# Performance work log

Measured on AMD Instinct MI355X. Metric: run time of the kernel, lower is better.

Reference implementation:

```python
import jax, jax.numpy as jnp
import numpy as np

B, L, D, NH, NITEMS = 256, 200, 128, 2, 100000
HD = D // NH
LAMB = 0.6
NEG = -1e9

_PARAM_SHAPES = dict(
    item_emb=(NITEMS, D), pos_emb=(L, D),
    W_ei=(D, D), b_ei=(D,), W_eo=(D, D), b_eo=(D,), b_iah=(D,), b_oah=(D,),
    w_ih=(3 * D, 2 * D), b_ih=(3 * D,), w_hh=(3 * D, D), b_hh=(3 * D,),
    ln1_g=(D,), ln1_b=(D,),
    Wq=(D, D), bq=(D,), Wk=(D, D), bk=(D,), Wv=(D, D), bv=(D,), Wo=(D, D), bo=(D,),
    ln2_g=(D,), ln2_b=(D,), W1=(D, D), b1=(D,), W2=(D, D), b2=(D,),
    lnf_g=(D,), lnf_b=(D,),
)


def setup_inputs() -> dict:
    key = jax.random.key(0)
    ks = jax.random.split(key, len(_PARAM_SHAPES) + 2)
    stdv = 1.0 / np.sqrt(D)  # GCSAN._init_weights: uniform(-stdv, stdv) on ALL params
    p = {}
    for i, (name, shp) in enumerate(_PARAM_SHAPES.items()):
        p[name] = jax.random.uniform(ks[i], shp, jnp.float32, -stdv, stdv)
    lens = jax.random.randint(ks[-2], (B,), L // 4, L + 1)
    vals = jax.random.randint(ks[-1], (B, L), 1, NITEMS)
    # trailing zero padding, as the original break-on-zero loop assumes
    seqs = jnp.where(jnp.arange(L)[None, :] < lens[:, None], vals, 0).astype(jnp.int32)
    p['seqs'] = seqs
    p['lens'] = lens.astype(jnp.int32)
    return p


def _ln(x, g, b):
    mu = x.mean(-1, keepdims=True)
    var = ((x - mu) ** 2).mean(-1, keepdims=True)
    return (x - mu) / jnp.sqrt(var + 1e-5) * g + b


def _build_graph(seqs):
    # Vectorized replacement of _get_slice (per-row np.unique + adjacency build)
    def per_row(seq):
        s = jnp.sort(seq)
        first = jnp.concatenate([jnp.ones((1,), bool), s[1:] != s[:-1]])
        pos = jnp.cumsum(first) - 1  # compaction target of each first-occurrence
        items = jnp.zeros((L,), seq.dtype).at[jnp.where(first, pos, L)].set(s, mode='drop')
        n_u = first.sum()
        search = jnp.where(jnp.arange(L) < n_u, items, jnp.iinfo(jnp.int32).max)
        alias = jnp.searchsorted(search, seq).astype(jnp.int32)
        return items, alias
    items, alias = jax.vmap(per_row)(seqs)
    valid = seqs[:, 1:] > 0  # edge (i -> i+1) exists until first pad
    u = jnp.where(valid, alias[:, :-1], L)  # route masked edges to dummy row L
    v = jnp.where(valid, alias[:, 1:], L)
    bidx = jnp.arange(B)[:, None]
    uA = jnp.zeros((B, L + 1, L + 1), jnp.float32).at[bidx, u, v].set(1.0)[:, :L, :L]
    in_deg = jnp.maximum(uA.sum(1), 1.0)
    out_deg = jnp.maximum(uA.sum(2), 1.0)
    A_in = jnp.swapaxes(uA, 1, 2) / in_deg[:, :, None]   # A[i,j] = uA[j,i]/in_deg[i]
    A_out = uA / out_deg[:, :, None]                     # A[i,k] = uA[i,k]/out_deg[i]
    return alias, jnp.concatenate([A_in, A_out], axis=2), items  # A: [B, L, 2L]


def reference(item_emb, pos_emb, W_ei, b_ei, W_eo, b_eo, b_iah, b_oah,
              w_ih, b_ih, w_hh, b_hh, ln1_g, ln1_b, Wq, bq, Wk, bk, Wv, bv,
              Wo, bo, ln2_g, ln2_b, W1, b1, W2, b2, lnf_g, lnf_b, seqs, lens):
    alias, A, items = _build_graph(seqs)
    hidden = item_emb[items]  # [B, L, D]
    # SR-GNN gated cell, step = n_layers = 1
    for _ in range(1):
        h_in = jnp.einsum('bij,bjd->bid', A[:, :, :L], hidden @ W_ei.T + b_ei) + b_iah
        h_out = jnp.einsum('bij,bjd->bid', A[:, :, L:], hidden @ W_eo.T + b_eo) + b_oah
        gi = jnp.concatenate([h_in, h_out], -1) @ w_ih.T + b_ih
        gh = hidden @ w_hh.T + b_hh
        i_r, i_i, i_n = jnp.split(gi, 3, -1)
        h_r, h_i, h_n = jnp.split(gh, 3, -1)
        r = jax.nn.sigmoid(i_r + h_r)
        z = jax.nn.sigmoid(i_i + h_i)
        ng = jnp.tanh(i_n + r * h_n)
        hidden = ng + z * (hidden - ng)
    bidx = jnp.arange(B)
    seq_hidden = hidden[bidx[:, None], alias]  # alias-gather back to sequence order
    last_idx = lens - 1
    ht = seq_hidden[bidx, last_idx]
    x = seq_hidden + pos_emb[None, :, :]
    tl_mask = (seqs > 0)[:, :, None].astype(x.dtype)
    x = x * tl_mask
    causal = jnp.triu(jnp.ones((L, L), bool), 1)  # True = masked future (bidirectional=False)
    # SASRec-style block: ln -> MHA residual -> ln -> pointwise FFN residual
    q_in = _ln(x, ln1_g, ln1_b)
    heads = lambda t: t.reshape(B, L, NH, HD).transpose(0, 2, 1, 3)
    q = heads(q_in @ Wq.T + bq)
    k = heads(x @ Wk.T + bk)
    v = heads(x @ Wv.T + bv)
    sc = jnp.einsum('bhqd,bhkd->bhqk', q, k) / jnp.sqrt(jnp.asarray(HD, x.dtype))
    sc = jnp.where(causal[None, None], NEG, sc)
    attn = jax.nn.softmax(sc, -1)
    mo = jnp.einsum('bhqk,bhkd->bhqd', attn, v).transpose(0, 2, 1, 3).reshape(B, L, D) @ Wo.T + bo
    x = q_in + mo
    h = _ln(x, ln2_g, ln2_b)
    x = h + jax.nn.relu(h @ W1.T + b1) @ W2.T + b2
    x = x * tl_mask
    log_feats = _ln(x, lnf_g, lnf_b)
    out = log_feats[bidx, last_idx]
    return LAMB * out + (1.0 - LAMB) * ht
```

## Files before the change

kernel.cpp:

```cpp
#include <hip/hip_runtime.h>
#include <hip/hip_bf16.h>

#define Bb 256
#define Ll 200
#define Dd 128
#define BL (Bb*Ll)
#define KVS 264

typedef __hip_bfloat16 bf16;
typedef __attribute__((ext_vector_type(8))) short short8;
typedef __attribute__((ext_vector_type(4))) unsigned short ushort4v;
typedef __attribute__((ext_vector_type(4))) float floatx4;

__device__ __forceinline__ float b2f(bf16 v) { return __bfloat162float(v); }
__device__ __forceinline__ bf16  f2b(float v) { return __float2bfloat16(v); }
__device__ __forceinline__ float us2f(unsigned short u) { return __uint_as_float(((unsigned)u) << 16); }
__device__ __forceinline__ unsigned short f2us(float v) { bf16 t = f2b(v); return *(unsigned short*)&t; }
__device__ __forceinline__ float ldf(const void* p, int i, int f32) {
  return f32 ? ((const float*)p)[i] : b2f(((const bf16*)p)[i]);
}
__device__ __forceinline__ int detect_f32(const unsigned short* __restrict__ w) {
  unsigned short u = w[threadIdx.x & 63];
  return (__ballot(((u >> 7) & 0xFF) >= 0x7F) != 0ull) ? 1 : 0;
}
__device__ __forceinline__ void load_lds16(const void* g, void* l) {
  __builtin_amdgcn_global_load_lds((const __attribute__((address_space(1))) unsigned int*)g,
                                   (__attribute__((address_space(3))) unsigned int*)l, 16, 0, 0);
}
__device__ __forceinline__ short8 emb_chunk8(const void* __restrict__ emb, int it, int g, int f32) {
  short8 o;
  if (f32) {
    const float4* e = (const float4*)((const float*)emb + (size_t)it * 128 + g * 8);
    float4 a = e[0], b = e[1];
    o[0] = (short)f2us(a.x); o[1] = (short)f2us(a.y); o[2] = (short)f2us(a.z); o[3] = (short)f2us(a.w);
    o[4] = (short)f2us(b.x); o[5] = (short)f2us(b.y); o[6] = (short)f2us(b.z); o[7] = (short)f2us(b.w);
  } else {
    o = ((const short8*)((const bf16*)emb + (size_t)it * 128))[g];
  }
  return o;
}

struct PackP {
  const void *W_ei,*W_eo,*w_ih,*w_hh,*Wk,*Wv,*Wqp,*Wop,*W1p,*W2p,*pos;
  const void *b_ei,*b_eo,*b_ih,*b_hh,*bk,*bv,*bqp,*bop,*b1p,*b2p,*biah,*boah;
  const void *ln1g,*ln1b,*ln2g,*ln2b,*lnfg,*lnfb;
  bf16 *cWhe,*cWih,*cWhh,*cWkv,*cWq,*cWo,*cW1,*cW2,*cPos;
  float *bias_he,*bias_gi,*bias_gh,*bias_kv,*cbq,*cbo,*cb1,*cb2,*cbiah,*cboah,*cln;
  const int* seqs;
  int *alias_g, *items_g; float *rin_g, *rout_g; unsigned *adj_g, *adjT_g;
};
__global__ __launch_bounds__(256) void k01(PackP p) {
  __shared__ alignas(16) int s[Ll];
  __shared__ int al[Ll], its[Ll];
  __shared__ alignas(4) unsigned char isf[Ll];
  __shared__ unsigned adjL[Ll*8], adjTL[Ll*8];
  if (blockIdx.x >= Bb) {
    int idx = (blockIdx.x - Bb) * 256 + threadIdx.x;
    int f32 = detect_f32((const unsigned short*)p.W_ei);
    if (idx < 131072) {
      if (idx < 32768) {
        int r = idx >> 7, c = idx & 127;
        p.cWhe[idx] = f2b(r < 128 ? ldf(p.W_ei, r*128+c, f32) : ldf(p.W_eo, (r-128)*128+c, f32));
      } else p.cWih[idx-32768] = f2b(ldf(p.w_ih, idx-32768, f32));
    } else if (idx < 278528) {
      if (idx < 180224)      p.cWhh[idx-131072] = f2b(ldf(p.w_hh, idx-131072, f32));
      else if (idx < 212992) {
        int i = idx - 180224; int r = i >> 7, c = i & 127;
        p.cWkv[i] = f2b(r < 128 ? ldf(p.Wk, r*128+c, f32) : ldf(p.Wv, (r-128)*128+c, f32));
      }
      else if (idx < 229376) p.cWq[idx-212992] = f2b(ldf(p.Wqp, idx-212992, f32));
      else if (idx < 245760) p.cWo[idx-229376] = f2b(ldf(p.Wop, idx-229376, f32));
      else if (idx < 262144) p.cW1[idx-245760] = f2b(ldf(p.W1p, idx-245760, f32));
      else                   p.cW2[idx-262144] = f2b(ldf(p.W2p, idx-262144, f32));
    } else if (idx < 304128) {
      p.cPos[idx-278528] = f2b(ldf(p.pos, idx-278528, f32));
    } else {
      int j = idx - 304128;
      if      (j < 256)  p.bias_he[j]     = (j<128) ? ldf(p.b_ei,j,f32) : ldf(p.b_eo,j-128,f32);
      else if (j < 640)  p.bias_gi[j-256] = ldf(p.b_ih, j-256, f32);
      else if (j < 1024) p.bias_gh[j-640] = ldf(p.b_hh, j-640, f32);
      else if (j < 1280) { int c=j-1024; p.bias_kv[c] = (c<128)? ldf(p.bk,c,f32): ldf(p.bv,c-128,f32); }
      else if (j < 1408) p.cbq[j-1280]   = ldf(p.bqp, j-1280, f32);
      else if (j < 1536) p.cbo[j-1408]   = ldf(p.bop, j-1408, f32);
      else if (j < 1664) p.cb1[j-1536]   = ldf(p.b1p, j-1536, f32);
      else if (j < 1792) p.cb2[j-1664]   = ldf(p.b2p, j-1664, f32);
      else if (j < 1920) p.cbiah[j-1792] = ldf(p.biah, j-1792, f32);
      else if (j < 2048) p.cboah[j-1920] = ldf(p.boah, j-1920, f32);
      else {
        int i = j - 2048, g = i >> 7, c2 = i & 127;
        const void* s6 = g==0?p.ln1g: g==1?p.ln1b: g==2?p.ln2g: g==3?p.ln2b: g==4?p.lnfg: p.lnfb;
        p.cln[i] = ldf(s6, c2, f32);
      }
    }
    return;
  }
  int b = blockIdx.x, t = threadIdx.x;
  if (t < Ll) s[t] = p.seqs[b*Ll + t];
  for (int i = t; i < Ll*8; i += 256) { adjL[i] = 0u; adjTL[i] = 0u; }
  __syncthreads();
  const int4* s4 = (const int4*)s;
  if (t < Ll) {
    int v = s[t]; int dup = 0;
    int nb = t >> 2;
    for (int j4 = 0; j4 < nb; j4++) {
      int4 sv = s4[j4];
      dup |= (sv.x==v) | (sv.y==v) | (sv.z==v) | (sv.w==v);
    }
    for (int j = nb*4; j < t; j++) dup |= (s[j]==v);
    isf[t] = dup ? 0 : 1; its[t] = 0;
  }
  __syncthreads();
  const unsigned* isfw = (const unsigned*)isf;
  if (t < Ll) {
    int v = s[t], r = 0;
    for (int j4 = 0; j4 < Ll/4; j4++) {
      int4 sv = s4[j4];
      unsigned fw = isfw[j4];
      r += ((fw & 0xffu)       && sv.x < v);
      r += ((fw & 0xff00u)     && sv.y < v);
      r += ((fw & 0xff0000u)   && sv.z < v);
      r += ((fw & 0xff000000u) && sv.w < v);
    }
    al[t] = r;
  }
  __syncthreads();
  if (t < Ll && isf[t]) its[al[t]] = s[t];
  if (t < Ll-1 && s[t+1] > 0) {
    int u = al[t], v = al[t+1];
    atomicOr(&adjL [u*8 + (v >> 5)], 1u << (v & 31));
    atomicOr(&adjTL[v*8 + (u >> 5)], 1u << (u & 31));
  }
  __syncthreads();
  if (t < Ll) {
    int od = 0, id = 0;
    for (int wd = 0; wd < 7; wd++) { od += __popc(adjL[t*8+wd]); id += __popc(adjTL[t*8+wd]); }
    p.rout_g [b*Ll + t] = 1.0f / (float)max(od, 1);
    p.rin_g  [b*Ll + t] = 1.0f / (float)max(id, 1);
    p.alias_g[b*Ll + t] = al[t];
    p.items_g[b*Ll + t] = its[t];
  }
  for (int i = t; i < Ll*8; i += 256) { p.adj_g[b*Ll*8 + i] = adjL[i]; p.adjT_g[b*Ll*8 + i] = adjTL[i]; }
}

__global__ __launch_bounds__(256) void gemm_he2(const void* __restrict__ emb, const int* __restrict__ items_g,
    const bf16* __restrict__ W, const float* __restrict__ bias,
    bf16* __restrict__ out_lo, int Nlo, bf16* __restrict__ out_hi, int Nhi, int split)
{
  __shared__ short As[128*128];
  __shared__ short Ws[128*128];
  int t = threadIdx.x;
  int wave = t >> 6, lane = t & 63;
  int q = lane >> 4, mr = lane & 15;
  int wm = wave & 1, wn = wave >> 1;
  int m0 = blockIdx.x * 128;
  int f32 = detect_f32((const unsigned short*)emb);
  {
    int r = t >> 1, half = t & 1;
    int it = items_g[m0 + r];
#pragma unroll
    for (int g8 = 0; g8 < 8; g8++) {
      int g = half*8 + g8;
      short8 o = emb_chunk8(emb, it, g, f32);
      *(short8*)&As[r*128 + (g ^ (r & 15))*8] = o;
    }
  }
  int srow = lane >> 4, c16 = lane & 15;
  for (int nt = 0; nt < 5; nt++) {
    int n0 = nt * 128;
#pragma unroll
    for (int i = 0; i < 8; i++) {
      int seg = wave*8 + i;
      int r = seg*4 + srow;
      int gch = c16 ^ (r & 15);
      load_lds16(W + (size_t)(n0 + r) * 128 + gch*8, &Ws[seg*512]);
    }
    __syncthreads();
    floatx4 acc[4][4] = {};
#pragma unroll
    for (int kk = 0; kk < 4; kk++) {
      short8 af[4], wf[4];
#pragma unroll
      for (int i = 0; i < 4; i++) {
        int row = wm*64 + i*16 + mr;
        af[i] = *(const short8*)(&As[row*128 + ((kk*4+q) ^ (row&15))*8]);
      }
#pragma unroll
      for (int j = 0; j < 4; j++) {
        int row = wn*64 + j*16 + mr;
        wf[j] = *(const short8*)(&Ws[row*128 + ((kk*4+q) ^ (row&15))*8]);
      }
#pragma unroll
      for (int i = 0; i < 4; i++)
#pragma unroll
        for (int j = 0; j < 4; j++)
          acc[i][j] = __builtin_amdgcn_mfma_f32_16x16x32_bf16(wf[j], af[i], acc[i][j], 0, 0, 0);
    }
#pragma unroll
    for (int j = 0; j < 4; j++) {
      int ng = n0 + wn*64 + j*16 + q*4;
      floatx4 bs = *(const floatx4*)(bias + ng);
      bf16* outp; int col, stride;
      if (ng < split) { outp = out_lo; col = ng; stride = Nlo; }
      else            { outp = out_hi; col = ng - split; stride = Nhi; }
#pragma unroll
      for (int i = 0; i < 4; i++) {
        int m = m0 + wm*64 + i*16 + mr;
        ushort4v o;
#pragma unroll
        for (int e = 0; e < 4; e++) o[e] = f2us(acc[i][j][e] + bs[e]);
        *(ushort4v*)(outp + (size_t)m * stride + col) = o;
      }
    }
    if (nt + 1 < 5) __syncthreads();
  }
}

template<int K>
__global__ __launch_bounds__(256) void gemm6(const bf16* __restrict__ A, const bf16* __restrict__ W,
    const float* __restrict__ bias,
    bf16* __restrict__ out_lo, int Nlo, bf16* __restrict__ out_hi, int Nhi, int split)
{
  __shared__ short As[128*128];
  __shared__ short Ws[128*128];
  int t = threadIdx.x;
  int wave = t >> 6, lane = t & 63;
  int q = lane >> 4, mr = lane & 15;
  int wm = wave & 1, wn = wave >> 1;
  int m0 = blockIdx.x * 128, n0 = blockIdx.y * 128;
  int srow = lane >> 4;
  int c16 = lane & 15;
  floatx4 acc[4][4] = {};
  for (int k0 = 0; k0 < K; k0 += 128) {
#pragma unroll
    for (int i = 0; i < 8; i++) {
      int seg = wave*8 + i;
      int r = seg*4 + srow;
      int gch = c16 ^ (r & 15);
      load_lds16(A + (size_t)(m0 + r) * K + k0 + gch*8, &As[seg*512]);
      load_lds16(W + (size_t)(n0 + r) * K + k0 + gch*8, &Ws[seg*512]);
    }
    __syncthreads();
#pragma unroll
    for (int kk = 0; kk < 4; kk++) {
      short8 af[4], wf[4];
#pragma unroll
      for (int i = 0; i < 4; i++) {
        int row = wm*64 + i*16 + mr;
        af[i] = *(const short8*)(&As[row*128 + ((kk*4+q) ^ (row&15))*8]);
      }
#pragma unroll
      for (int j = 0; j < 4; j++) {
        int row = wn*64 + j*16 + mr;
        wf[j] = *(const short8*)(&Ws[row*128 + ((kk*4+q) ^ (row&15))*8]);
      }
#pragma unroll
      for (int i = 0; i < 4; i++)
#pragma unroll
        for (int j = 0; j < 4; j++)
          acc[i][j] = __builtin_amdgcn_mfma_f32_16x16x32_bf16(wf[j], af[i], acc[i][j], 0, 0, 0);
    }
    if (k0 + 128 < K) __syncthreads();
  }
#pragma unroll
  for (int j = 0; j < 4; j++) {
    int ng = n0 + wn*64 + j*16 + q*4;
    floatx4 bs = *(const floatx4*)(bias + ng);
    bf16* outp; int col, stride;
    if (ng < split) { outp = out_lo; col = ng; stride = Nlo; }
    else            { outp = out_hi; col = ng - split; stride = Nhi; }
#pragma unroll
    for (int i = 0; i < 4; i++) {
      int m = m0 + wm*64 + i*16 + mr;
      ushort4v o;
#pragma unroll
      for (int e = 0; e < 4; e++) o[e] = f2us(acc[i][j][e] + bs[e]);
      *(ushort4v*)(outp + (size_t)m * stride + col) = o;
    }
  }
}

__global__ __launch_bounds__(256) void k3_agg(const bf16* __restrict__ he,
    const unsigned* __restrict__ adj_g, const unsigned* __restrict__ adjT_g,
    const float* __restrict__ rin_g, const float* __restrict__ rout_g,
    const float* __restrict__ cbiah, const float* __restrict__ cboah, bf16* __restrict__ hio)
{
  int b = blockIdx.x / 25, chunk = blockIdx.x % 25;
  int wave = threadIdx.x >> 6, lane = threadIdx.x & 63;
  bool isIn = lane < 32;
  int c = isIn ? 4*lane : 128 + 4*(lane-32);
  const bf16* heb = he + (size_t)b * Ll * 256;
  bf16* hiob = hio + (size_t)b * Ll * 256;
  float bias0 = isIn ? cbiah[c]   : cboah[c-128];
  float bias1 = isIn ? cbiah[c+1] : cboah[c-127];
  float bias2 = isIn ? cbiah[c+2] : cboah[c-126];
  float bias3 = isIn ? cbiah[c+3] : cboah[c-125];
#pragma unroll
  for (int s = 0; s < 2; s++) {
    int i = chunk*8 + wave + 4*s;
    const unsigned* mrow = (isIn ? adjT_g : adj_g) + ((size_t)b*Ll + i) * 8;
    float a0=0.f, a1=0.f, a2=0.f, a3=0.f;
    for (int wd = 0; wd < 7; wd++) {
      unsigned bits = mrow[wd];
      while (bits) {
        int j = (wd << 5) + __builtin_ctz(bits); bits &= bits - 1;
        ushort4v h4 = *(const ushort4v*)(heb + (size_t)j*256 + c);
        a0 += us2f(h4.x); a1 += us2f(h4.y); a2 += us2f(h4.z); a3 += us2f(h4.w);
      }
    }
    float r = isIn ? rin_g[b*Ll + i] : rout_g[b*Ll + i];
    ushort4v o;
    o.x = f2us(bias0 + r*a0); o.y = f2us(bias1 + r*a1);
    o.z = f2us(bias2 + r*a2); o.w = f2us(bias3 + r*a3);
    *(ushort4v*)(hiob + (size_t)i*256 + c) = o;
  }
}

struct KAP {
  const bf16 *gi, *gh; const void* emb; const int* seqs; const int* alias_g; const int* lens;
  const bf16 *cPos, *cWkv; const float* bias_kv;
  const bf16 *cWq, *cWo, *cW1, *cW2;
  const float *cbq, *cbo, *cb1, *cb2, *cln;
  void* out;
};
__device__ __forceinline__ float dot128i(const bf16* __restrict__ wrow, const float* __restrict__ vin) {
  const short8* wr = (const short8*)wrow;
  float a0=0.f, a1=0.f, a2=0.f, a3=0.f;
#pragma unroll
  for (int kk = 0; kk < 4; kk++) {
    short8 w0 = wr[kk*4+0], w1 = wr[kk*4+1], w2 = wr[kk*4+2], w3 = wr[kk*4+3];
#pragma unroll
    for (int j = 0; j < 8; j++) {
      a0 += vin[kk*32 +      j] * us2f((unsigned short)w0[j]);
      a1 += vin[kk*32 + 8  + j] * us2f((unsigned short)w1[j]);
      a2 += vin[kk*32 + 16 + j] * us2f((unsigned short)w2[j]);
      a3 += vin[kk*32 + 24 + j] * us2f((unsigned short)w3[j]);
    }
  }
  return (a0+a1)+(a2+a3);
}
__device__ __forceinline__ float wave_sum(float v) {
#pragma unroll
  for (int m = 1; m < 64; m <<= 1) v += __shfl_xor(v, m, 64);
  return v;
}
__device__ __forceinline__ float wave_max(float v) {
#pragma unroll
  for (int m = 1; m < 64; m <<= 1) v = fmaxf(v, __shfl_xor(v, m, 64));
  return v;
}
__global__ __launch_bounds__(256) void kv_attn(KAP p)
{
  __shared__ __align__(16) char pool[162688];
  short* xs   = (short*)pool;
  short* kvL  = (short*)(pool + 56576);
  float* htL  = (float*)(pool + 56576 + 105600);
  int* aliasL = (int*)(pool + 56576);
  int* seqL   = aliasL + 200;
  float* qin  = (float*)pool;
  float* qv   = qin + 128;
  float* aout = qv + 128;
  float* hh   = aout + 128;
  float* f1   = hh + 128;
  float* pb0  = f1 + 128;
  float* pb1  = pb0 + 256;
  floatx4* av4 = (floatx4*)(pb1 + 256);
  float* sred = (float*)(av4 + 8*32);

  int b = blockIdx.x, t = threadIdx.x;
  int wave = t >> 6, lane = t & 63, q = lane >> 4, mr = lane & 15;
  int li = p.lens[b] - 1;
  int f32 = detect_f32((const unsigned short*)p.emb);
  if (t < Ll) { aliasL[t] = p.alias_g[b*Ll + t]; seqL[t] = p.seqs[b*Ll + t]; }
  for (int u = t; u < 8*136; u += 256) xs[Ll*136 + u] = 0;
  __syncthreads();
  for (int u = t; u < Ll*16; u += 256) {
    int tpos = u >> 4, jv = u & 15;
    int a = aliasL[tpos];
    int it = seqL[tpos];
    const short8* gin = (const short8*)(p.gi + ((size_t)b*Ll + a) * 384);
    const short8* ghn = (const short8*)(p.gh + ((size_t)b*Ll + a) * 384);
    short8 vir = gin[jv], vii = gin[16+jv], vnn = gin[32+jv];
    short8 whr = ghn[jv], whi = ghn[16+jv], whn = ghn[32+jv];
    short8 hv  = emb_chunk8(p.emb, it, jv, f32);
    short8 pv  = ((const short8*)(p.cPos + tpos * Dd))[jv];
    bool isLast = (tpos == li);
    short8 o;
#pragma unroll
    for (int e = 0; e < 8; e++) {
      float ir = us2f((unsigned short)vir[e]), ii = us2f((unsigned short)vii[e]), inn = us2f((unsigned short)vnn[e]);
      float hr = us2f((unsigned short)whr[e]), hi = us2f((unsigned short)whi[e]), hn = us2f((unsigned short)whn[e]);
      float r  = 1.f / (1.f + __expf(-(ir + hr)));
      float z  = 1.f / (1.f + __expf(-(ii + hi)));
      float arg = inn + r * hn;
      float ex = __expf(-2.f * arg);
      float ng = (1.f - ex) / (1.f + ex);
      float h  = us2f((unsigned short)hv[e]);
      float sh = ng + z * (h - ng);
      o[e] = (short)f2us(sh + us2f((unsigned short)pv[e]));
      if (isLast) htL[jv*8 + e] = sh;
    }
    *(short8*)&xs[tpos*136 + jv*8] = o;
  }
  __syncthreads();
  {
    short8 wf[4][4];
#pragma unroll
    for (int kk = 0; kk < 4; kk++)
#pragma unroll
      for (int j = 0; j < 4; j++) {
        int n = wave*64 + j*16 + mr;
        wf[kk][j] = *(const short8*)(p.cWkv + (size_t)n*128 + kk*32 + q*8);
      }
    for (int mt = 0; mt < 13; mt++) {
      short8 af[4];
#pragma unroll
      for (int kk = 0; kk < 4; kk++)
        af[kk] = *(const short8*)&xs[(mt*16 + mr)*136 + (kk*4+q)*8];
      floatx4 acc[4] = {};
#pragma unroll
      for (int kk = 0; kk < 4; kk++)
#pragma unroll
        for (int j = 0; j < 4; j++)
          acc[j] = __builtin_amdgcn_mfma_f32_16x16x32_bf16(wf[kk][j], af[kk], acc[j], 0, 0, 0);
      int m = mt*16 + mr;
      if (m < Ll) {
#pragma unroll
        for (int j = 0; j < 4; j++) {
          int n = wave*64 + j*16 + q*4;
          floatx4 bs = *(const floatx4*)(p.bias_kv + n);
          ushort4v o;
#pragma unroll
          for (int e = 0; e < 4; e++) o[e] = f2us(acc[j][e] + bs[e]);
          *(ushort4v*)&kvL[m*KVS + n] = o;
        }
      }
    }
  }
  __syncthreads();
  int c = t, w = wave, ln = lane;
  float xv = (c < 128) ? (htL[c] + b2f(p.cPos[li*Dd + c])) : 0.f;
  float s = wave_sum(xv), s2 = wave_sum(xv*xv);
  if (ln == 0) { sred[w] = s; sred[4+w] = s2; }
  __syncthreads();
  float mu = (sred[0]+sred[1]+sred[2]+sred[3]) * (1.f/128.f);
  float ms = (sred[4]+sred[5]+sred[6]+sred[7]) * (1.f/128.f);
  float rs = rsqrtf(fmaxf(ms - mu*mu, 0.f) + 1e-5f);
  __syncthreads();
  if (c < 128) qin[c] = (xv - mu) * rs * p.cln[c] + p.cln[128+c];
  __syncthreads();
  if (c < 128) qv[c] = p.cbq[c] + dot128i(p.cWq + c*128, qin);
  __syncthreads();
  float s0 = -3.0e38f, s1 = -3.0e38f;
  if (t <= li) {
    const short8* kr = (const short8*)&kvL[t*KVS];
    float a00=0.f,a01=0.f,a10=0.f,a11=0.f;
#pragma unroll
    for (int kk = 0; kk < 4; kk++) {
      short8 k0 = kr[kk*2], k1 = kr[kk*2+1], k2 = kr[8+kk*2], k3 = kr[8+kk*2+1];
#pragma unroll
      for (int j = 0; j < 8; j++) {
        a00 += qv[kk*16 + j]      * us2f((unsigned short)k0[j]);
        a01 += qv[kk*16 + 8 + j]  * us2f((unsigned short)k1[j]);
        a10 += qv[64 + kk*16 + j]     * us2f((unsigned short)k2[j]);
        a11 += qv[64 + kk*16 + 8 + j] * us2f((unsigned short)k3[j]);
      }
    }
    s0 = (a00+a01) * 0.125f; s1 = (a10+a11) * 0.125f;
  }
  float m0 = wave_max(s0), m1 = wave_max(s1);
  if (ln == 0) { sred[w] = m0; sred[4+w] = m1; }
  __syncthreads();
  m0 = fmaxf(fmaxf(sred[0],sred[1]), fmaxf(sred[2],sred[3]));
  m1 = fmaxf(fmaxf(sred[4],sred[5]), fmaxf(sred[6],sred[7]));
  __syncthreads();
  float e0 = (t <= li) ? __expf(s0 - m0) : 0.f;
  float e1 = (t <= li) ? __expf(s1 - m1) : 0.f;
  pb0[t] = e0; pb1[t] = e1;
  float l0 = wave_sum(e0), l1 = wave_sum(e1);
  if (ln == 0) { sred[w] = l0; sred[4+w] = l1; }
  __syncthreads();
  l0 = sred[0]+sred[1]+sred[2]+sred[3];
  l1 = sred[4]+sred[5]+sred[6]+sred[7];
  {
    int part = t >> 5, cq = t & 31, ch = cq * 4;
    int cnt = li + 1, cpp = (cnt + 7) >> 3;
    int j0 = part * cpp, j1 = min(j0 + cpp, cnt);
    const float* pbh = (ch < 64) ? pb0 : pb1;
    float a0=0.f,a1=0.f,a2=0.f,a3=0.f;
#pragma unroll 4
    for (int j = j0; j < j1; j++) {
      ushort4v v4 = *(const ushort4v*)&kvL[j*KVS + 128 + ch];
      float pw = pbh[j];
      a0 += pw*us2f(v4.x); a1 += pw*us2f(v4.y); a2 += pw*us2f(v4.z); a3 += pw*us2f(v4.w);
    }
    floatx4 o = {a0,a1,a2,a3};
    av4[part*32 + cq] = o;
  }
  __syncthreads();
  if (c < 128) {
    float l = (c < 64) ? l0 : l1;
    float acc = 0.f;
#pragma unroll
    for (int pp = 0; pp < 8; pp++) acc += ((const float*)&av4[pp*32 + (c>>2)])[c&3];
    aout[c] = acc / l;
  }
  __syncthreads();
  float x2v = 0.f;
  if (c < 128) x2v = qin[c] + p.cbo[c] + dot128i(p.cWo + c*128, aout);
  s = wave_sum((c<128)?x2v:0.f); s2 = wave_sum((c<128)?x2v*x2v:0.f);
  if (ln == 0) { sred[w] = s; sred[4+w] = s2; }
  __syncthreads();
  mu = (sred[0]+sred[1]+sred[2]+sred[3]) * (1.f/128.f);
  ms = (sred[4]+sred[5]+sred[6]+sred[7]) * (1.f/128.f);
  rs = rsqrtf(fmaxf(ms - mu*mu, 0.f) + 1e-5f);
  __syncthreads();
  if (c < 128) hh[c] = (x2v - mu) * rs * p.cln[256+c] + p.cln[384+c];
  __syncthreads();
  if (c < 128) f1[c] = fmaxf(p.cb1[c] + dot128i(p.cW1 + c*128, hh), 0.f);
  __syncthreads();
  float x3v = 0.f;
  if (c < 128) x3v = hh[c] + p.cb2[c] + dot128i(p.cW2 + c*128, f1);
  s = wave_sum((c<128)?x3v:0.f); s2 = wave_sum((c<128)?x3v*x3v:0.f);
  if (ln == 0) { sred[w] = s; sred[4+w] = s2; }
  __syncthreads();
  mu = (sred[0]+sred[1]+sred[2]+sred[3]) * (1.f/128.f);
  ms = (sred[4]+sred[5]+sred[6]+sred[7]) * (1.f/128.f);
  rs = rsqrtf(fmaxf(ms - mu*mu, 0.f) + 1e-5f);
  if (c < 128) {
    float lf = (x3v - mu) * rs * p.cln[512+c] + p.cln[640+c];
    float outv = 0.6f * lf + 0.4f * htL[c];
    if (f32) ((float*)p.out)[b*Dd + c] = outv;
    else     ((bf16*)p.out)[b*Dd + c]  = f2b(outv);
  }
}

extern "C" void kernel_launch(void* const* d_in, const int* in_sizes, int n_in,
                              void* d_out, int out_size, void* d_ws, size_t ws_size,
                              hipStream_t stream)
{
  (void)in_sizes; (void)n_in; (void)out_size; (void)ws_size;
  const void* item_emb = d_in[0];
  const int* seqs = (const int*)d_in[30];
  const int* lens = (const int*)d_in[31];

  char* wsp = (char*)d_ws;
  size_t o = 0;
  auto alloc = [&](size_t sz) { void* p = wsp + o; o += (sz + 255) & ~(size_t)255; return p; };
  int*      alias_g = (int*)alloc((size_t)BL*4);
  int*      items_g = (int*)alloc((size_t)BL*4);
  float*    rin_g   = (float*)alloc((size_t)BL*4);
  float*    rout_g  = (float*)alloc((size_t)BL*4);
  unsigned* adj_g   = (unsigned*)alloc((size_t)BL*8*4);
  unsigned* adjT_g  = (unsigned*)alloc((size_t)BL*8*4);
  bf16*     cWhe    = (bf16*)alloc(32768*2);
  bf16*     cWhh    = (bf16*)alloc(49152*2);
  bf16*     cWih    = (bf16*)alloc(98304*2);
  bf16*     cWkv    = (bf16*)alloc(32768*2);
  bf16*     cWq     = (bf16*)alloc(16384*2);
  bf16*     cWo     = (bf16*)alloc(16384*2);
  bf16*     cW1     = (bf16*)alloc(16384*2);
  bf16*     cW2     = (bf16*)alloc(16384*2);
  bf16*     cPos    = (bf16*)alloc(25600*2);
  float*    bias_he = (float*)alloc(256*4);
  float*    bias_gh = (float*)alloc(384*4);
  float*    bias_gi = (float*)alloc(384*4);
  float*    bias_kv = (float*)alloc(256*4);
  float*    cbq     = (float*)alloc(128*4);
  float*    cbo     = (float*)alloc(128*4);
  float*    cb1     = (float*)alloc(128*4);
  float*    cb2     = (float*)alloc(128*4);
  float*    cbiah   = (float*)alloc(128*4);
  float*    cboah   = (float*)alloc(128*4);
  float*    cln     = (float*)alloc(768*4);
  bf16*     he      = (bf16*)alloc((size_t)BL*256*2);
  bf16*     hio     = (bf16*)alloc((size_t)BL*256*2);
  bf16*     gi      = (bf16*)alloc((size_t)BL*384*2);
  bf16*     gh      = (bf16*)alloc((size_t)BL*384*2);

  PackP pp = { d_in[2], d_in[4], d_in[8], d_in[10], d_in[16], d_in[18], d_in[14], d_in[20],
               d_in[24], d_in[26], d_in[1],
               d_in[3], d_in[5], d_in[9], d_in[11], d_in[17], d_in[19], d_in[15], d_in[21],
               d_in[25], d_in[27], d_in[6], d_in[7],
               d_in[12], d_in[13], d_in[22], d_in[23], d_in[28], d_in[29],
               cWhe, cWih, cWhh, cWkv, cWq, cWo, cW1, cW2, cPos,
               bias_he, bias_gi, bias_gh, bias_kv, cbq, cbo, cb1, cb2, cbiah, cboah, cln,
               seqs, alias_g, items_g, rin_g, rout_g, adj_g, adjT_g };
  k01<<<Bb + 1199, 256, 0, stream>>>(pp);
  gemm_he2<<<BL/128, 256, 0, stream>>>(item_emb, items_g, cWhe, bias_he, he, 256, gh, 384, 256);
  k3_agg<<<Bb*25, 256, 0, stream>>>(he, adj_g, adjT_g, rin_g, rout_g, cbiah, cboah, hio);
  gemm6<256><<<dim3(BL/128, 3), 256, 0, stream>>>(hio, cWih, bias_gi, gi, 384, gi, 384, 1<<30);
  KAP kp = { gi, gh, item_emb, seqs, alias_g, lens, cPos, cWkv, bias_kv,
             cWq, cWo, cW1, cW2, cbq, cbo, cb1, cb2, cln, d_out };
  kv_attn<<<Bb, 256, 0, stream>>>(kp);
}
```

Before: 259.5 us.

## Double kv_attn block to 512 threads and split KV GEMM rows across waves

Launches the per-sequence attention kernel with 512 threads instead of 256. The two halves of the block now take different M-tile ranges of the K/V projection MFMA loop, and the value accumulation is split into 16 partitions. Block reductions are rewritten for 8 waves through a helper that does an extra barrier per statistic. Since the large LDS footprint limits the kernel to one block per CU, the aim is more in-flight waves to hide latency, at the cost of extra barriers and idle threads in the 128-wide tail phases.

Measured after the change: 260.1 us. Within noise of the previous version (+0.2%).

```diff
diff --git a/kernel.cpp b/kernel.cpp
--- a/kernel.cpp
+++ b/kernel.cpp
@@ -348,7 +348,16 @@
   for (int m = 1; m < 64; m <<= 1) v = fmaxf(v, __shfl_xor(v, m, 64));
   return v;
 }
-__global__ __launch_bounds__(256) void kv_attn(KAP p)
+__device__ __forceinline__ float blk_sum8(float v, float* sred, int w, int ln, int slot) {
+  float s = wave_sum(v);
+  if (ln == 0) sred[slot*8 + w] = s;
+  __syncthreads();
+  float r = 0.f;
+#pragma unroll
+  for (int i = 0; i < 8; i++) r += sred[slot*8 + i];
+  return r;
+}
+__global__ __launch_bounds__(512) void kv_attn(KAP p)
 {
   __shared__ __align__(16) char pool[162688];
   short* xs   = (short*)pool;
@@ -364,16 +373,16 @@
   float* pb0  = f1 + 128;
   float* pb1  = pb0 + 256;
   floatx4* av4 = (floatx4*)(pb1 + 256);
-  float* sred = (float*)(av4 + 8*32);
+  float* sred = (float*)(av4 + 16*32);
 
   int b = blockIdx.x, t = threadIdx.x;
   int wave = t >> 6, lane = t & 63, q = lane >> 4, mr = lane & 15;
   int li = p.lens[b] - 1;
   int f32 = detect_f32((const unsigned short*)p.emb);
   if (t < Ll) { aliasL[t] = p.alias_g[b*Ll + t]; seqL[t] = p.seqs[b*Ll + t]; }
-  for (int u = t; u < 8*136; u += 256) xs[Ll*136 + u] = 0;
-  __syncthreads();
-  for (int u = t; u < Ll*16; u += 256) {
+  for (int u = t; u < 8*136; u += 512) xs[Ll*136 + u] = 0;
+  __syncthreads();
+  for (int u = t; u < Ll*16; u += 512) {
     int tpos = u >> 4, jv = u & 15;
     int a = aliasL[tpos];
     int it = seqL[tpos];
@@ -403,15 +412,17 @@
   }
   __syncthreads();
   {
+    int nq = wave & 3, hf = wave >> 2;
     short8 wf[4][4];
 #pragma unroll
     for (int kk = 0; kk < 4; kk++)
 #pragma unroll
       for (int j = 0; j < 4; j++) {
-        int n = wave*64 + j*16 + mr;
+        int n = nq*64 + j*16 + mr;
         wf[kk][j] = *(const short8*)(p.cWkv + (size_t)n*128 + kk*32 + q*8);
       }
-    for (int mt = 0; mt < 13; mt++) {
+    int mtBeg = hf ? 7 : 0, mtEnd = hf ? 13 : 7;
+    for (int mt = mtBeg; mt < mtEnd; mt++) {
       short8 af[4];
 #pragma unroll
       for (int kk = 0; kk < 4; kk++)
@@ -426,7 +437,7 @@
       if (m < Ll) {
 #pragma unroll
         for (int j = 0; j < 4; j++) {
-          int n = wave*64 + j*16 + q*4;
+          int n = nq*64 + j*16 + q*4;
           floatx4 bs = *(const floatx4*)(p.bias_kv + n);
           ushort4v o;
 #pragma unroll
@@ -439,11 +450,10 @@
   __syncthreads();
   int c = t, w = wave, ln = lane;
   float xv = (c < 128) ? (htL[c] + b2f(p.cPos[li*Dd + c])) : 0.f;
-  float s = wave_sum(xv), s2 = wave_sum(xv*xv);
-  if (ln == 0) { sred[w] = s; sred[4+w] = s2; }
-  __syncthreads();
-  float mu = (sred[0]+sred[1]+sred[2]+sred[3]) * (1.f/128.f);
-  float ms = (sred[4]+sred[5]+sred[6]+sred[7]) * (1.f/128.f);
+  float sa = blk_sum8(xv, sred, w, ln, 0);
+  float sb = blk_sum8(xv*xv, sred, w, ln, 1);
+  float mu = sa * (1.f/128.f);
+  float ms = sb * (1.f/128.f);
   float rs = rsqrtf(fmaxf(ms - mu*mu, 0.f) + 1e-5f);
   __syncthreads();
   if (c < 128) qin[c] = (xv - mu) * rs * p.cln[c] + p.cln[128+c];
@@ -468,22 +478,20 @@
     s0 = (a00+a01) * 0.125f; s1 = (a10+a11) * 0.125f;
   }
   float m0 = wave_max(s0), m1 = wave_max(s1);
-  if (ln == 0) { sred[w] = m0; sred[4+w] = m1; }
-  __syncthreads();
-  m0 = fmaxf(fmaxf(sred[0],sred[1]), fmaxf(sred[2],sred[3]));
-  m1 = fmaxf(fmaxf(sred[4],sred[5]), fmaxf(sred[6],sred[7]));
+  if (ln == 0) { sred[w] = m0; sred[8+w] = m1; }
+  __syncthreads();
+  m0 = sred[0]; m1 = sred[8];
+#pragma unroll
+  for (int i = 1; i < 8; i++) { m0 = fmaxf(m0, sred[i]); m1 = fmaxf(m1, sred[8+i]); }
   __syncthreads();
   float e0 = (t <= li) ? __expf(s0 - m0) : 0.f;
   float e1 = (t <= li) ? __expf(s1 - m1) : 0.f;
-  pb0[t] = e0; pb1[t] = e1;
-  float l0 = wave_sum(e0), l1 = wave_sum(e1);
-  if (ln == 0) { sred[w] = l0; sred[4+w] = l1; }
-  __syncthreads();
-  l0 = sred[0]+sred[1]+sred[2]+sred[3];
-  l1 = sred[4]+sred[5]+sred[6]+sred[7];
+  if (t < 256) { pb0[t] = e0; pb1[t] = e1; }
+  float l0 = blk_sum8(e0, sred, w, ln, 0);
+  float l1 = blk_sum8(e1, sred, w, ln, 1);
   {
     int part = t >> 5, cq = t & 31, ch = cq * 4;
-    int cnt = li + 1, cpp = (cnt + 7) >> 3;
+    int cnt = li + 1, cpp = (cnt + 15) >> 4;
     int j0 = part * cpp, j1 = min(j0 + cpp, cnt);
     const float* pbh = (ch < 64) ? pb0 : pb1;
     float a0=0.f,a1=0.f,a2=0.f,a3=0.f;
@@ -501,17 +509,15 @@
     float l = (c < 64) ? l0 : l1;
     float acc = 0.f;
 #pragma unroll
-    for (int pp = 0; pp < 8; pp++) acc += ((const float*)&av4[pp*32 + (c>>2)])[c&3];
+    for (int pp = 0; pp < 16; pp++) acc += ((const float*)&av4[pp*32 + (c>>2)])[c&3];
     aout[c] = acc / l;
   }
   __syncthreads();
   float x2v = 0.f;
   if (c < 128) x2v = qin[c] + p.cbo[c] + dot128i(p.cWo + c*128, aout);
-  s = wave_sum((c<128)?x2v:0.f); s2 = wave_sum((c<128)?x2v*x2v:0.f);
-  if (ln == 0) { sred[w] = s; sred[4+w] = s2; }
-  __syncthreads();
-  mu = (sred[0]+sred[1]+sred[2]+sred[3]) * (1.f/128.f);
-  ms = (sred[4]+sred[5]+sred[6]+sred[7]) * (1.f/128.f);
+  sa = blk_sum8((c<128)?x2v:0.f, sred, w, ln, 0);
+  sb = blk_sum8((c<128)?x2v*x2v:0.f, sred, w, ln, 1);
+  mu = sa * (1.f/128.f); ms = sb * (1.f/128.f);
   rs = rsqrtf(fmaxf(ms - mu*mu, 0.f) + 1e-5f);
   __syncthreads();
   if (c < 128) hh[c] = (x2v - mu) * rs * p.cln[256+c] + p.cln[384+c];
@@ -520,11 +526,9 @@
   __syncthreads();
   float x3v = 0.f;
   if (c < 128) x3v = hh[c] + p.cb2[c] + dot128i(p.cW2 + c*128, f1);
-  s = wave_sum((c<128)?x3v:0.f); s2 = wave_sum((c<128)?x3v*x3v:0.f);
-  if (ln == 0) { sred[w] = s; sred[4+w] = s2; }
-  __syncthreads();
-  mu = (sred[0]+sred[1]+sred[2]+sred[3]) * (1.f/128.f);
-  ms = (sred[4]+sred[5]+sred[6]+sred[7]) * (1.f/128.f);
+  sa = blk_sum8((c<128)?x3v:0.f, sred, w, ln, 0);
+  sb = blk_sum8((c<128)?x3v*x3v:0.f, sred, w, ln, 1);
+  mu = sa * (1.f/128.f); ms = sb * (1.f/128.f);
   rs = rsqrtf(fmaxf(ms - mu*mu, 0.f) + 1e-5f);
   if (c < 128) {
     float lf = (x3v - mu) * rs * p.cln[512+c] + p.cln[640+c];
@@ -591,5 +595,5 @@
   gemm6<256><<<dim3(BL/128, 3), 256, 0, stream>>>(hio, cWih, bias_gi, gi, 384, gi, 384, 1<<30);
   KAP kp = { gi, gh, item_emb, seqs, alias_g, lens, cPos, cWkv, bias_kv,
              cWq, cWo, cW1, cW2, cbq, cbo, cb1, cb2, cln, d_out };
-  kv_attn<<<Bb, 256, 0, stream>>>(kp);
-}
+  kv_attn<<<Bb, 512, 0, stream>>>(kp);
+}
```
